# Kernel optimization log

Hardware: AMD Instinct MI355X
Metric: run time of the kernel (lower is better)

The kernel has to match this reference:

```python
import jax, jax.numpy as jnp
import numpy as np

EMBED = 512
HEADS = 8
FMUL = 4
TAU = 2.0
V_TH = 1.0      # spiking threshold (spikingjelly default)
ALPHA = 2.0     # ATan surrogate alpha (spikingjelly default)
EPS = 1e-5


@jax.custom_vjp
def spike_fn(v):
    # Heaviside spike with ATan surrogate gradient (spikingjelly surrogate.ATan)
    return (v >= V_TH).astype(v.dtype)

def _spike_fwd(v):
    return spike_fn(v), v

def _spike_bwd(v, g):
    t = (jnp.pi / 2.0) * ALPHA * (v - V_TH)
    return (g * (ALPHA / 2.0) / (1.0 + t * t),)

spike_fn.defvjp(_spike_fwd, _spike_bwd)


def layernorm(x, g, b):
    mu = jnp.mean(x, axis=-1, keepdims=True)
    var = jnp.mean(jnp.square(x - mu), axis=-1, keepdims=True)
    return (x - mu) * jax.lax.rsqrt(var + EPS) * g + b


def setup_inputs() -> dict:
    key = jax.random.key(0)
    ks = jax.random.split(key, 12)
    m, s, e = 4, 2048, EMBED
    f = e * FMUL
    sc = 0.02
    return {
        "x":  jax.random.normal(ks[0], (m, s, e), jnp.float32),
        "wq": jax.random.normal(ks[1], (e, e), jnp.float32) * sc,
        "bq": jnp.zeros((e,), jnp.float32),
        "wk": jax.random.normal(ks[2], (e, e), jnp.float32) * sc,
        "bk": jnp.zeros((e,), jnp.float32),
        "wv": jax.random.normal(ks[3], (e, e), jnp.float32) * sc,
        "bv": jnp.zeros((e,), jnp.float32),
        "w1": jax.random.normal(ks[4], (e, f), jnp.float32) * sc,
        "b1": jnp.zeros((f,), jnp.float32),
        "w2": jax.random.normal(ks[5], (f, e), jnp.float32) * sc,
        "b2": jnp.zeros((e,), jnp.float32),
        "g1": jnp.ones((e,), jnp.float32),
        "be1": jnp.zeros((e,), jnp.float32),
        "g2": jnp.ones((e,), jnp.float32),
        "be2": jnp.zeros((e,), jnp.float32),
    }


def reference(x, wq, bq, wk, bk, wv, bv, w1, b1, w2, b2, g1, be1, g2, be2):
    m, s, e = x.shape
    h = HEADS
    d = e // h

    # --- pre-norm attention (NOTE: original has NO 1/sqrt(d) scaling) ---
    n1 = layernorm(x, g1, be1)
    q = (n1 @ wq + bq).reshape(m, s, h, d).transpose(0, 2, 1, 3)  # [m,h,s,d]
    k = (n1 @ wk + bk).reshape(m, s, h, d).transpose(0, 2, 1, 3)
    v = (n1 @ wv + bv).reshape(m, s, h, d).transpose(0, 2, 1, 3)
    scores = jnp.einsum('bhqd,bhkd->bhqk', q, k)       # [m,h,s,s], unscaled
    attn = jax.nn.softmax(scores, axis=-1)
    ctx = jnp.einsum('bhqk,bhkd->bhqd', attn, v)       # [m,h,s,d]
    att_out = ctx.transpose(0, 2, 1, 3).reshape(m, s, e)

    x = x + att_out
    # dropout p=0.4 is identity at inference (eval path in the original)

    # --- FFN with spiking activation ---
    n2 = layernorm(x, g2, be2)
    h1 = n2 @ w1 + b1                                  # [m,s,4e]
    # single-step LIF charge from v=0: v = v + (x - v)/tau = x/tau
    spikes = spike_fn(h1 / TAU)
    return x + (spikes @ w2 + b2)
```

## Files before the change

### kernel.cpp

```cpp
#include <hip/hip_runtime.h>
#include <stdint.h>

#define EMB 512
#define SEQ 2048
#define MB 4
#define NH 8
#define HD 64
#define ROWS (MB*SEQ)
#define MARGIN 0.02f
#define CAP 65536
#define LOG2E 1.44269504f
#define EXPB (-17.3123405f)

typedef unsigned short u16;
typedef __attribute__((ext_vector_type(8))) short bf16x8;
typedef __attribute__((ext_vector_type(4))) float f32x4;
typedef __attribute__((ext_vector_type(2))) unsigned int u32x2;
typedef __attribute__((ext_vector_type(4))) unsigned int u32x4;

union Frag { u32x2 u[2]; bf16x8 v; };
union Frag4 { unsigned u[4]; bf16x8 v; };

__device__ __forceinline__ u16 f2bf(float f) {
  union { float f; unsigned u; } a; a.f = f;
  unsigned r = a.u + 0x7FFFu + ((a.u >> 16) & 1u);
  return (u16)(r >> 16);
}
__device__ __forceinline__ float bflo(unsigned u) {
  union { unsigned u; float f; } c; c.u = u << 16; return c.f;
}
__device__ __forceinline__ float bfhi(unsigned u) {
  union { unsigned u; float f; } c; c.u = u & 0xffff0000u; return c.f;
}
__device__ __forceinline__ void gld16(const void* g, void* l) {
  __builtin_amdgcn_global_load_lds(
      (const __attribute__((address_space(1))) void*)g,
      (__attribute__((address_space(3))) void*)l, 16, 0, 0);
}


__global__ __launch_bounds__(256) void k_prep(
    const float* __restrict__ x, const float* __restrict__ g1, const float* __restrict__ be1,
    const float* __restrict__ wq, const float* __restrict__ wk,
    const float* __restrict__ wv, const float* __restrict__ w1,
    u16* __restrict__ n1, u16* __restrict__ wqkvT, u16* __restrict__ w1T,
    int* __restrict__ cnt) {
  __shared__ float tile[32][33];
  int b = blockIdx.x, tid = threadIdx.x;
  if (b < 1792) {
    const float* src; u16* dst; int N, bx, by;
    if (b < 768) {
      int z = b >> 8, rem = b & 255; bx = rem & 15; by = rem >> 4; N = 512;
      src = (z == 0) ? wq : ((z == 1) ? wk : wv);
      dst = wqkvT + z * 512 * 512;
    } else {
      int rem = b - 768; bx = rem & 63; by = rem >> 6; N = 2048;
      src = w1; dst = w1T;
    }
    int tx = tid & 31, ty = tid >> 5;
    int k0 = by * 32, n0 = bx * 32;
    for (int i = 0; i < 32; i += 8)
      tile[ty + i][tx] = src[(size_t)(k0 + ty + i) * N + n0 + tx];
    __syncthreads();
    for (int i = 0; i < 32; i += 8)
      dst[(size_t)(n0 + ty + i) * 512 + k0 + tx] = f2bf(tile[tx][ty + i]);
  } else {
    if (b == 1792 && tid < 2) cnt[tid] = 0;
    int wid = tid >> 6, lane = tid & 63;
    int row = (b - 1792) * 4 + wid;
    const float* xr = x + (size_t)row * EMB + lane * 8;
    f32x4 v0 = *(const f32x4*)xr;
    f32x4 v1 = *(const f32x4*)(xr + 4);
    float s = v0.x+v0.y+v0.z+v0.w + v1.x+v1.y+v1.z+v1.w;
    float q = v0.x*v0.x+v0.y*v0.y+v0.z*v0.z+v0.w*v0.w
            + v1.x*v1.x+v1.y*v1.y+v1.z*v1.z+v1.w*v1.w;
    #pragma unroll
    for (int o = 1; o < 64; o <<= 1) { s += __shfl_xor(s, o); q += __shfl_xor(q, o); }
    float mu = s * (1.0f/512.0f);
    float rs = 1.0f / sqrtf(q * (1.0f/512.0f) - mu*mu + 1e-5f);
    f32x4 ga = *(const f32x4*)(g1 + lane*8), gb = *(const f32x4*)(g1 + lane*8 + 4);
    f32x4 ba = *(const f32x4*)(be1 + lane*8), bb = *(const f32x4*)(be1 + lane*8 + 4);
    union { u16 h[8]; u32x4 v; } o8;
    o8.h[0] = f2bf((v0.x-mu)*rs*ga.x + ba.x); o8.h[1] = f2bf((v0.y-mu)*rs*ga.y + ba.y);
    o8.h[2] = f2bf((v0.z-mu)*rs*ga.z + ba.z); o8.h[3] = f2bf((v0.w-mu)*rs*ga.w + ba.w);
    o8.h[4] = f2bf((v1.x-mu)*rs*gb.x + bb.x); o8.h[5] = f2bf((v1.y-mu)*rs*gb.y + bb.y);
    o8.h[6] = f2bf((v1.z-mu)*rs*gb.z + bb.z); o8.h[7] = f2bf((v1.w-mu)*rs*gb.w + bb.w);
    *(u32x4*)(n1 + (size_t)row * EMB + lane * 8) = o8.v;
  }
}

__global__ __launch_bounds__(256) void k_ln2(const float* __restrict__ x,
    const u16* __restrict__ att, const float* __restrict__ g, const float* __restrict__ b,
    const float* __restrict__ b2, float* __restrict__ x2, u16* __restrict__ n2,
    float* __restrict__ out) {
  int wid = threadIdx.x >> 6, lane = threadIdx.x & 63;
  int row = blockIdx.x * 4 + wid;
  size_t base = (size_t)row * EMB + lane * 8;
  u32x4 av = *(const u32x4*)(att + base);
  f32x4 t0, t1;
  t0.x = bflo(av.x); t0.y = bfhi(av.x); t0.z = bflo(av.y); t0.w = bfhi(av.y);
  t1.x = bflo(av.z); t1.y = bfhi(av.z); t1.z = bflo(av.w); t1.w = bfhi(av.w);
  f32x4 v0 = *(const f32x4*)(x + base)     + t0;
  f32x4 v1 = *(const f32x4*)(x + base + 4) + t1;
  *(f32x4*)(x2 + base) = v0;
  *(f32x4*)(x2 + base + 4) = v1;
  *(f32x4*)(out + base)     = v0 + *(const f32x4*)(b2 + lane*8);
  *(f32x4*)(out + base + 4) = v1 + *(const f32x4*)(b2 + lane*8 + 4);
  float s = v0.x+v0.y+v0.z+v0.w + v1.x+v1.y+v1.z+v1.w;
  float q = v0.x*v0.x+v0.y*v0.y+v0.z*v0.z+v0.w*v0.w
          + v1.x*v1.x+v1.y*v1.y+v1.z*v1.z+v1.w*v1.w;
  #pragma unroll
  for (int o = 1; o < 64; o <<= 1) { s += __shfl_xor(s, o); q += __shfl_xor(q, o); }
  float mu = s * (1.0f/512.0f);
  float rs = 1.0f / sqrtf(q * (1.0f/512.0f) - mu*mu + 1e-5f);
  f32x4 ga = *(const f32x4*)(g + lane*8), gb = *(const f32x4*)(g + lane*8 + 4);
  f32x4 ba = *(const f32x4*)(b + lane*8), bb = *(const f32x4*)(b + lane*8 + 4);
  union { u16 h[8]; u32x4 v; } o8;
  o8.h[0] = f2bf((v0.x-mu)*rs*ga.x + ba.x); o8.h[1] = f2bf((v0.y-mu)*rs*ga.y + ba.y);
  o8.h[2] = f2bf((v0.z-mu)*rs*ga.z + ba.z); o8.h[3] = f2bf((v0.w-mu)*rs*ga.w + ba.w);
  o8.h[4] = f2bf((v1.x-mu)*rs*gb.x + bb.x); o8.h[5] = f2bf((v1.y-mu)*rs*gb.y + bb.y);
  o8.h[6] = f2bf((v1.z-mu)*rs*gb.z + bb.z); o8.h[7] = f2bf((v1.w-mu)*rs*gb.w + bb.w);
  *(u32x4*)(n2 + (size_t)row * EMB + lane * 8) = o8.v;
}

#define GEMM_CORE(A_, Bt_, m0_, n0_)                                           \
  __shared__ u16 As[2][128 * 32];                                              \
  __shared__ u16 Bs[2][128 * 32];                                              \
  int tid = threadIdx.x;                                                       \
  int wid = tid >> 6, lane = tid & 63;                                         \
  int quad = lane >> 4, ln15 = lane & 15;                                      \
  int wm = (wid >> 1) * 64, wn = (wid & 1) * 64;                               \
  int arow = lane >> 2, acol = (lane & 3) * 8;                                 \
  const u16* gA0 = A_  + (size_t)(m0_ + wid * 32 + arow) * 512 + acol;         \
  const u16* gA1 = gA0 + (size_t)16 * 512;                                     \
  const u16* gB0 = Bt_ + (size_t)(n0_ + wid * 32 + arow) * 512 + acol;         \
  const u16* gB1 = gB0 + (size_t)16 * 512;                                     \
  f32x4 acc[4][4] = {};                                                        \
  gld16(gA0, &As[0][(wid * 32) * 32]); gld16(gA1, &As[0][(wid * 32 + 16) * 32]);\
  gld16(gB0, &Bs[0][(wid * 32) * 32]); gld16(gB1, &Bs[0][(wid * 32 + 16) * 32]);\
  for (int kt = 0; kt < 16; kt++) {                                            \
    int cur = kt & 1;                                                          \
    __syncthreads();                                                           \
    if (kt < 15) {                                                             \
      int ko = (kt + 1) * 32;                                                  \
      gld16(gA0 + ko, &As[cur ^ 1][(wid * 32) * 32]);                          \
      gld16(gA1 + ko, &As[cur ^ 1][(wid * 32 + 16) * 32]);                     \
      gld16(gB0 + ko, &Bs[cur ^ 1][(wid * 32) * 32]);                          \
      gld16(gB1 + ko, &Bs[cur ^ 1][(wid * 32 + 16) * 32]);                     \
    }                                                                          \
    bf16x8 af[4], bf[4];                                                       \
    _Pragma("unroll")                                                          \
    for (int i = 0; i < 4; i++) {                                              \
      af[i] = *(const bf16x8*)&As[cur][(wm + i * 16 + ln15) * 32 + quad * 8];  \
      bf[i] = *(const bf16x8*)&Bs[cur][(wn + i * 16 + ln15) * 32 + quad * 8];  \
    }                                                                          \
    _Pragma("unroll")                                                          \
    for (int i = 0; i < 4; i++)                                                \
      _Pragma("unroll")                                                        \
      for (int j = 0; j < 4; j++)                                              \
        acc[i][j] = __builtin_amdgcn_mfma_f32_16x16x32_bf16(af[i], bf[j],      \
                                                            acc[i][j], 0, 0, 0);\
  }                                                                            \
  __syncthreads();

__global__ __launch_bounds__(256) void k_gemm_qkv(
    const u16* __restrict__ A, const u16* __restrict__ Bt,
    const float* __restrict__ bq, const float* __restrict__ bk, const float* __restrict__ bv,
    u16* __restrict__ Qb, u16* __restrict__ Kb, u16* __restrict__ Vtb) {
  int bid = blockIdx.x + 12 * blockIdx.y;
  int c = bid & 7, r = bid >> 3;
  int m0 = (c * 8 + r / 12) * 128, n0 = (r % 12) * 128;
  GEMM_CORE(A, Bt, m0, n0)
  #pragma unroll
  for (int j = 0; j < 4; j++) {
    int n = n0 + wn + j * 16 + ln15;
    int t = n >> 9, cc = n & 511, head = cc >> 6, dd = cc & 63;
    float bias = (t == 0) ? bq[cc] : ((t == 1) ? bk[cc] : bv[cc]);
    #pragma unroll
    for (int i = 0; i < 4; i++) {
      int row0 = m0 + wm + i * 16 + quad * 4;
      int mm = row0 >> 11, ss0 = row0 & 2047;
      if (t == 2) {
        union { u16 h[4]; u32x2 v; } pk;
        #pragma unroll
        for (int r2 = 0; r2 < 4; r2++) pk.h[r2] = f2bf(acc[i][j][r2] + bias);
        *(u32x2*)(Vtb + ((size_t)(mm * 8 + head) * 64 + dd) * 2048 + ss0) = pk.v;
      } else {
        u16* dst = (t == 0) ? Qb : Kb;
        #pragma unroll
        for (int r2 = 0; r2 < 4; r2++)
          dst[((size_t)(mm * 8 + head) * 2048 + ss0 + r2) * 64 + dd] =
              f2bf(acc[i][j][r2] + bias);
      }
    }
  }
}

__global__ __launch_bounds__(256) void k_gemm_ffn1(
    const u16* __restrict__ A, const u16* __restrict__ Bt, const float* __restrict__ b1,
    int* __restrict__ cnt, unsigned* __restrict__ spikeL, unsigned* __restrict__ candL) {
  int bid = blockIdx.x + 16 * blockIdx.y;
  int c = bid & 7, r = bid >> 3;
  int m0 = (c * 8 + r / 16) * 128, n0 = (r % 16) * 128;
  GEMM_CORE(A, Bt, m0, n0)
  #pragma unroll
  for (int j = 0; j < 4; j++) {
    int n = n0 + wn + j * 16 + ln15;
    float bias = b1[n];
    #pragma unroll
    for (int i = 0; i < 4; i++) {
      #pragma unroll
      for (int r2 = 0; r2 < 4; r2++) {
        int row = m0 + wm + i * 16 + quad * 4 + r2;
        float hv = acc[i][j][r2] + bias;
        if (hv >= 2.0f - MARGIN) {
          if (hv >= 2.0f + MARGIN) {
            int ix = atomicAdd(&cnt[0], 1);
            if (ix < CAP) spikeL[ix] = (unsigned)(row * 2048 + n);
          } else {
            int ix = atomicAdd(&cnt[1], 1);
            if (ix < CAP) candL[ix] = (unsigned)(row * 2048 + n);
          }
        }
      }
    }
  }
}

#define F_STAGE(BUF, T0)                                                       \
  do {                                                                         \
    gld16(gK0 + (size_t)(T0)       * 4096, &L.SB[BUF][0][0][rb0 * 64]);        \
    gld16(gK1 + (size_t)(T0)       * 4096, &L.SB[BUF][0][0][rb1 * 64]);        \
    gld16(gK0 + (size_t)((T0) + 1) * 4096, &L.SB[BUF][0][1][rb0 * 64]);        \
    gld16(gK1 + (size_t)((T0) + 1) * 4096, &L.SB[BUF][0][1][rb1 * 64]);        \
    gld16(gV0 + (T0) * 64,       &L.SB[BUF][1][0][rb0 * 64]);                  \
    gld16(gV1 + (T0) * 64,       &L.SB[BUF][1][0][rb1 * 64]);                  \
    gld16(gV0 + ((T0) + 1) * 64, &L.SB[BUF][1][1][rb0 * 64]);                  \
    gld16(gV1 + ((T0) + 1) * 64, &L.SB[BUF][1][1][rb1 * 64]);                  \
  } while (0)

#define F_INNER(BUF, SUB)                                                      \
  do {                                                                         \
    const u16* Kc = L.SB[BUF][0][SUB];                                         \
    const u16* Vc = L.SB[BUF][1][SUB];                                         \
    f32x4 s4[2][4];                                                            \
    __builtin_amdgcn_s_setprio(1);                                             \
    _Pragma("unroll")                                                          \
    for (int j = 0; j < 4; j++) {                                              \
      bf16x8 a = *(const bf16x8*)(Kc + (j * 16 + ln15) * 64 + ((quad ^ lm) * 8)); \
      s4[0][j] = __builtin_amdgcn_mfma_f32_16x16x32_bf16(a, aQ[0][0].v, z4, 0, 0, 0); \
      s4[1][j] = __builtin_amdgcn_mfma_f32_16x16x32_bf16(a, aQ[1][0].v, z4, 0, 0, 0); \
    }                                                                          \
    _Pragma("unroll")                                                          \
    for (int j = 0; j < 4; j++) {                                              \
      bf16x8 a = *(const bf16x8*)(Kc + (j * 16 + ln15) * 64 + (((4 + quad) ^ lm) * 8)); \
      s4[0][j] = __builtin_amdgcn_mfma_f32_16x16x32_bf16(a, aQ[0][1].v, s4[0][j], 0, 0, 0); \
      s4[1][j] = __builtin_amdgcn_mfma_f32_16x16x32_bf16(a, aQ[1][1].v, s4[1][j], 0, 0, 0); \
    }                                                                          \
    __builtin_amdgcn_s_setprio(0);                                             \
    Frag4 bP[2][2];                                                            \
    _Pragma("unroll")                                                          \
    for (int h = 0; h < 2; h++) {                                              \
      unsigned pr[4][4];                                                       \
      _Pragma("unroll")                                                        \
      for (int j = 0; j < 4; j++)                                              \
        _Pragma("unroll")                                                      \
        for (int r = 0; r < 4; r++) {                                          \
          float p = __builtin_amdgcn_exp2f(fmaf(s4[h][j][r], LOG2E, EXPB));    \
          union { float f; unsigned u; } cc; cc.f = p;                         \
          pr[j][r] = cc.u;                                                     \
        }                                                                      \
      _Pragma("unroll")                                                        \
      for (int t = 0; t < 2; t++) {                                            \
        bP[h][t].u[0] = __builtin_amdgcn_perm(pr[2*t][1],   pr[2*t][0],   0x07060302u); \
        bP[h][t].u[1] = __builtin_amdgcn_perm(pr[2*t][3],   pr[2*t][2],   0x07060302u); \
        bP[h][t].u[2] = __builtin_amdgcn_perm(pr[2*t+1][1], pr[2*t+1][0], 0x07060302u); \
        bP[h][t].u[3] = __builtin_amdgcn_perm(pr[2*t+1][3], pr[2*t+1][2], 0x07060302u); \
      }                                                                        \
    }                                                                          \
    __builtin_amdgcn_s_setprio(1);                                             \
    lacc[0] = __builtin_amdgcn_mfma_f32_16x16x32_bf16(vOne.v, bP[0][0].v, lacc[0], 0, 0, 0); \
    lacc[1] = __builtin_amdgcn_mfma_f32_16x16x32_bf16(vOne.v, bP[1][0].v, lacc[1], 0, 0, 0); \
    lacc[0] = __builtin_amdgcn_mfma_f32_16x16x32_bf16(vOne.v, bP[0][1].v, lacc[0], 0, 0, 0); \
    lacc[1] = __builtin_amdgcn_mfma_f32_16x16x32_bf16(vOne.v, bP[1][1].v, lacc[1], 0, 0, 0); \
    _Pragma("unroll")                                                          \
    for (int t = 0; t < 2; t++)                                                \
      _Pragma("unroll")                                                        \
      for (int j = 0; j < 4; j++) {                                            \
        int row = j * 16 + ln15;                                               \
        int c0 = 4 * t + (quad >> 1), sub = (quad & 1) * 4;                    \
        Frag aV;                                                               \
        aV.u[0] = *(const u32x2*)(Vc + row * 64 + ((c0 ^ lm) * 8) + sub);      \
        aV.u[1] = *(const u32x2*)(Vc + row * 64 + (((c0 + 2) ^ lm) * 8) + sub);\
        U[0][j] = __builtin_amdgcn_mfma_f32_16x16x32_bf16(aV.v, bP[0][t].v,    \
                                                          U[0][j], 0, 0, 0);   \
        U[1][j] = __builtin_amdgcn_mfma_f32_16x16x32_bf16(aV.v, bP[1][t].v,    \
                                                          U[1][j], 0, 0, 0);   \
      }                                                                        \
    __builtin_amdgcn_s_setprio(0);                                             \
  } while (0)

#define F_STEP(CUR, S)                                                         \
  do {                                                                         \
    __syncthreads();                                                           \
    if ((S) < 15) F_STAGE((CUR) ^ 1, 2 * (S) + 2);                             \
    F_INNER(CUR, 0);                                                           \
    F_INNER(CUR, 1);                                                           \
  } while (0)

__global__ __launch_bounds__(256, 2) void k_flash(
    const u16* __restrict__ Q, const u16* __restrict__ K,
    const u16* __restrict__ Vt, u16* __restrict__ att) {
  __shared__ union {
    u16 SB[2][2][2][64 * 64];
    float T[4][16 * 68];
  } L;
  int tid = threadIdx.x, wid = tid >> 6, lane = tid & 63;
  int quad = lane >> 4, ln15 = lane & 15, lm = ln15 & 7;
  int bid = blockIdx.x + 16 * (blockIdx.y + 8 * (int)blockIdx.z);
  int swz = (bid & 7) * 64 + (bid >> 3);
  int qb = swz & 15, head = (swz >> 4) & 7, mm = swz >> 7;
  int mh = mm * 8 + head;
  const u16* Qp = Q  + (size_t)mh * SEQ * HD;
  const u16* Kp = K  + (size_t)mh * SEQ * HD;
  const u16* Vp = Vt + (size_t)mh * HD * SEQ;
  int q0 = qb * 128 + wid * 32;

  Frag aQ[2][2];
  #pragma unroll
  for (int h = 0; h < 2; h++)
    #pragma unroll
    for (int t = 0; t < 2; t++) {
      u32x4 g = *(const u32x4*)(Qp + (size_t)(q0 + h * 16 + ln15) * 64 + t * 32 + quad * 8);
      aQ[h][t].u[0].x = g.x; aQ[h][t].u[0].y = g.y;
      aQ[h][t].u[1].x = g.z; aQ[h][t].u[1].y = g.w;
    }
  const f32x4 z4 = {0.f, 0.f, 0.f, 0.f};
  Frag4 vOne;
  vOne.u[0] = 0x3F803F80u; vOne.u[1] = 0x3F803F80u;
  vOne.u[2] = 0x3F803F80u; vOne.u[3] = 0x3F803F80u;

  int srow = lane >> 3;
  int sch  = (lane & 7) ^ (srow & 7);
  int rb0 = wid * 16, rb1 = wid * 16 + 8;
  const u16* gK0 = Kp + (size_t)(rb0 + srow) * 64 + sch * 8;
  const u16* gK1 = Kp + (size_t)(rb1 + srow) * 64 + sch * 8;
  const u16* gV0 = Vp + (size_t)(rb0 + srow) * SEQ + sch * 8;
  const u16* gV1 = Vp + (size_t)(rb1 + srow) * SEQ + sch * 8;

  f32x4 lacc[2] = {};
  f32x4 U[2][4] = {};

  F_STAGE(0, 0);
  for (int it = 0; it < 8; it++) {
    F_STEP(0, 2 * it);
    F_STEP(1, 2 * it + 1);
  }
  __syncthreads();

  #pragma unroll
  for (int h = 0; h < 2; h++) {
    float rl = 1.0f / lacc[h][0];
    float* Tw = L.T[wid];
    #pragma unroll
    for (int j = 0; j < 4; j++)
      *(f32x4*)(Tw + ln15 * 68 + j * 16 + quad * 4) = U[h][j] * rl;
    #pragma unroll
    for (int s = 0; s < 4; s++) {
      f32x4 o = *(const f32x4*)(Tw + (quad * 4 + s) * 68 + ln15 * 4);
      union { u16 h4[4]; u32x2 v; } pk;
      pk.h4[0] = f2bf(o.x); pk.h4[1] = f2bf(o.y);
      pk.h4[2] = f2bf(o.z); pk.h4[3] = f2bf(o.w);
      *(u32x2*)(att + ((size_t)mm * SEQ + q0 + h * 16 + quad * 4 + s) * EMB +
                head * 64 + ln15 * 4) = pk.v;
    }
  }
}

__global__ __launch_bounds__(256) void k_fixup(
    const float* __restrict__ x2, const float* __restrict__ w1, const float* __restrict__ b1,
    const float* __restrict__ g2, const float* __restrict__ be2,
    int* __restrict__ cnt, unsigned* __restrict__ spikeL, const unsigned* __restrict__ candL) {
  __shared__ float sb[8];
  int tid = threadIdx.x;
  int nC = cnt[1]; if (nC > CAP) nC = CAP;
  for (int e = blockIdx.x; e < nC; e += gridDim.x) {
    unsigned v = candL[e];
    int row = (int)(v >> 11), col = (int)(v & 2047u);
    const float* xr = x2 + (size_t)row * 512;
    float x0 = xr[tid], x1 = xr[tid + 256];
    float s = x0 + x1, q = x0 * x0 + x1 * x1;
    #pragma unroll
    for (int o = 1; o < 64; o <<= 1) { s += __shfl_xor(s, o); q += __shfl_xor(q, o); }
    if ((tid & 63) == 0) { sb[tid >> 6] = s; sb[4 + (tid >> 6)] = q; }
    __syncthreads();
    float st = sb[0] + sb[1] + sb[2] + sb[3];
    float qt = sb[4] + sb[5] + sb[6] + sb[7];
    __syncthreads();
    float mu = st * (1.f / 512.f);
    float rs = 1.f / sqrtf(qt * (1.f / 512.f) - mu * mu + 1e-5f);
    float na = (x0 - mu) * rs * g2[tid] + be2[tid];
    float nb = (x1 - mu) * rs * g2[tid + 256] + be2[tid + 256];
    float dd = na * w1[(size_t)tid * 2048 + col] + nb * w1[(size_t)(tid + 256) * 2048 + col];
    #pragma unroll
    for (int o = 1; o < 64; o <<= 1) dd += __shfl_xor(dd, o);
    if ((tid & 63) == 0) sb[tid >> 6] = dd;
    __syncthreads();
    if (tid == 0) {
      float hv = sb[0] + sb[1] + sb[2] + sb[3] + b1[col];
      if (hv >= 2.0f) { int ix = atomicAdd(&cnt[0], 1); if (ix < CAP) spikeL[ix] = v; }
    }
    __syncthreads();
  }
}

__global__ void k_apply(const float* __restrict__ w2, const int* __restrict__ cnt,
                        const unsigned* __restrict__ spikeL, float* __restrict__ out) {
  int n = cnt[0]; if (n > CAP) n = CAP;
  int tid = threadIdx.x;
  for (int e = blockIdx.x; e < n; e += gridDim.x) {
    unsigned v = spikeL[e];
    int row = (int)(v >> 11), col = (int)(v & 2047u);
    atomicAdd(&out[(size_t)row * 512 + tid * 2 + 0], w2[(size_t)col * 512 + tid * 2 + 0]);
    atomicAdd(&out[(size_t)row * 512 + tid * 2 + 1], w2[(size_t)col * 512 + tid * 2 + 1]);
  }
}


extern "C" void kernel_launch(void* const* d_in, const int* in_sizes, int n_in,
                              void* d_out, int out_size, void* d_ws, size_t ws_size,
                              hipStream_t stream) {
  (void)in_sizes; (void)n_in; (void)out_size; (void)ws_size;
  const float* x   = (const float*)d_in[0];
  const float* wq  = (const float*)d_in[1];
  const float* bq  = (const float*)d_in[2];
  const float* wk  = (const float*)d_in[3];
  const float* bk  = (const float*)d_in[4];
  const float* wv  = (const float*)d_in[5];
  const float* bv  = (const float*)d_in[6];
  const float* w1  = (const float*)d_in[7];
  const float* b1  = (const float*)d_in[8];
  const float* w2  = (const float*)d_in[9];
  const float* b2  = (const float*)d_in[10];
  const float* g1  = (const float*)d_in[11];
  const float* be1 = (const float*)d_in[12];
  const float* g2  = (const float*)d_in[13];
  const float* be2 = (const float*)d_in[14];
  float* out = (float*)d_out;

  char* w = (char*)d_ws;
  size_t off = 0;
  auto take = [&](size_t bytes) { char* p = w + off; off += (bytes + 255) & ~(size_t)255; return p; };
  int*      cnt    = (int*)take(256);
  u16*      n1     = (u16*)take((size_t)ROWS * EMB * 2);
  u16*      wqkvT  = (u16*)take((size_t)1536 * 512 * 2);
  u16*      w1T    = (u16*)take((size_t)2048 * 512 * 2);
  u16*      Qb     = (u16*)take((size_t)MB * NH * SEQ * HD * 2);
  u16*      Kb     = (u16*)take((size_t)MB * NH * SEQ * HD * 2);
  u16*      Vtb    = (u16*)take((size_t)MB * NH * SEQ * HD * 2);
  u16*      att    = (u16*)take((size_t)ROWS * EMB * 2);
  float*    x2     = (float*)take((size_t)ROWS * EMB * 4);
  u16*      n2     = (u16*)take((size_t)ROWS * EMB * 2);
  unsigned* spikeL = (unsigned*)take((size_t)CAP * 4);
  unsigned* candL  = (unsigned*)take((size_t)CAP * 4);

  k_prep<<<3840, 256, 0, stream>>>(x, g1, be1, wq, wk, wv, w1, n1, wqkvT, w1T, cnt);
  k_gemm_qkv<<<dim3(12, 64), 256, 0, stream>>>(n1, wqkvT, bq, bk, bv, Qb, Kb, Vtb);
  k_flash<<<dim3(16, 8, 4), 256, 0, stream>>>(Qb, Kb, Vtb, att);
  k_ln2<<<ROWS / 4, 256, 0, stream>>>(x, att, g2, be2, b2, x2, n2, out);
  k_gemm_ffn1<<<dim3(16, 64), 256, 0, stream>>>(n2, w1T, b1, cnt, spikeL, candL);
  k_fixup<<<256, 256, 0, stream>>>(x2, w1, b1, g2, be2, cnt, spikeL, candL);
  k_apply<<<128, 256, 0, stream>>>(w2, cnt, spikeL, out);
}
```

Measured before the change: 199.1 us.

## Fold log2e into K weights and exp bias into MFMA accumulator; drop x2 buffer

Scales the K projection weights and bias by log2(e) during prep, and seeds the QK^T MFMA accumulator with the constant exp offset. The softmax exponent then becomes a bare exp2 with no per-element FMA. Separately, k_ln2 no longer writes the fp32 residual x2; the fixup kernel recomputes it from x plus the bf16 attention output. This removes one full-size fp32 store at the cost of extra loads in the sparse fixup. Scaling K before bf16 rounding changes rounding slightly.

```diff
diff --git a/kernel.cpp b/kernel.cpp
--- a/kernel.cpp
+++ b/kernel.cpp
@@ -32,6 +32,9 @@
 __device__ __forceinline__ float bfhi(unsigned u) {
   union { unsigned u; float f; } c; c.u = u & 0xffff0000u; return c.f;
 }
+__device__ __forceinline__ float b2f(u16 h) {
+  union { unsigned u; float f; } c; c.u = (unsigned)h << 16; return c.f;
+}
 __device__ __forceinline__ void gld16(const void* g, void* l) {
   __builtin_amdgcn_global_load_lds(
       (const __attribute__((address_space(1))) void*)g,
@@ -49,9 +52,11 @@
   int b = blockIdx.x, tid = threadIdx.x;
   if (b < 1792) {
     const float* src; u16* dst; int N, bx, by;
+    float scl = 1.0f;
     if (b < 768) {
       int z = b >> 8, rem = b & 255; bx = rem & 15; by = rem >> 4; N = 512;
       src = (z == 0) ? wq : ((z == 1) ? wk : wv);
+      if (z == 1) scl = LOG2E;
       dst = wqkvT + z * 512 * 512;
     } else {
       int rem = b - 768; bx = rem & 63; by = rem >> 6; N = 2048;
@@ -63,7 +68,7 @@
       tile[ty + i][tx] = src[(size_t)(k0 + ty + i) * N + n0 + tx];
     __syncthreads();
     for (int i = 0; i < 32; i += 8)
-      dst[(size_t)(n0 + ty + i) * 512 + k0 + tx] = f2bf(tile[tx][ty + i]);
+      dst[(size_t)(n0 + ty + i) * 512 + k0 + tx] = f2bf(tile[tx][ty + i] * scl);
   } else {
     if (b == 1792 && tid < 2) cnt[tid] = 0;
     int wid = tid >> 6, lane = tid & 63;
@@ -91,7 +96,7 @@
 
 __global__ __launch_bounds__(256) void k_ln2(const float* __restrict__ x,
     const u16* __restrict__ att, const float* __restrict__ g, const float* __restrict__ b,
-    const float* __restrict__ b2, float* __restrict__ x2, u16* __restrict__ n2,
+    const float* __restrict__ b2, u16* __restrict__ n2,
     float* __restrict__ out) {
   int wid = threadIdx.x >> 6, lane = threadIdx.x & 63;
   int row = blockIdx.x * 4 + wid;
@@ -102,8 +107,6 @@
   t1.x = bflo(av.z); t1.y = bfhi(av.z); t1.z = bflo(av.w); t1.w = bfhi(av.w);
   f32x4 v0 = *(const f32x4*)(x + base)     + t0;
   f32x4 v1 = *(const f32x4*)(x + base + 4) + t1;
-  *(f32x4*)(x2 + base) = v0;
-  *(f32x4*)(x2 + base + 4) = v1;
   *(f32x4*)(out + base)     = v0 + *(const f32x4*)(b2 + lane*8);
   *(f32x4*)(out + base + 4) = v1 + *(const f32x4*)(b2 + lane*8 + 4);
   float s = v0.x+v0.y+v0.z+v0.w + v1.x+v1.y+v1.z+v1.w;
@@ -175,7 +178,7 @@
   for (int j = 0; j < 4; j++) {
     int n = n0 + wn + j * 16 + ln15;
     int t = n >> 9, cc = n & 511, head = cc >> 6, dd = cc & 63;
-    float bias = (t == 0) ? bq[cc] : ((t == 1) ? bk[cc] : bv[cc]);
+    float bias = (t == 0) ? bq[cc] : ((t == 1) ? bk[cc] * LOG2E : bv[cc]);
     #pragma unroll
     for (int i = 0; i < 4; i++) {
       int row0 = m0 + wm + i * 16 + quad * 4;
@@ -248,8 +251,8 @@
     _Pragma("unroll")                                                          \
     for (int j = 0; j < 4; j++) {                                              \
       bf16x8 a = *(const bf16x8*)(Kc + (j * 16 + ln15) * 64 + ((quad ^ lm) * 8)); \
-      s4[0][j] = __builtin_amdgcn_mfma_f32_16x16x32_bf16(a, aQ[0][0].v, z4, 0, 0, 0); \
-      s4[1][j] = __builtin_amdgcn_mfma_f32_16x16x32_bf16(a, aQ[1][0].v, z4, 0, 0, 0); \
+      s4[0][j] = __builtin_amdgcn_mfma_f32_16x16x32_bf16(a, aQ[0][0].v, e4, 0, 0, 0); \
+      s4[1][j] = __builtin_amdgcn_mfma_f32_16x16x32_bf16(a, aQ[1][0].v, e4, 0, 0, 0); \
     }                                                                          \
     _Pragma("unroll")                                                          \
     for (int j = 0; j < 4; j++) {                                              \
@@ -266,7 +269,7 @@
       for (int j = 0; j < 4; j++)                                              \
         _Pragma("unroll")                                                      \
         for (int r = 0; r < 4; r++) {                                          \
-          float p = __builtin_amdgcn_exp2f(fmaf(s4[h][j][r], LOG2E, EXPB));    \
+          float p = __builtin_amdgcn_exp2f(s4[h][j][r]);                       \
           union { float f; unsigned u; } cc; cc.f = p;                         \
           pr[j][r] = cc.u;                                                     \
         }                                                                      \
@@ -335,7 +338,7 @@
       aQ[h][t].u[0].x = g.x; aQ[h][t].u[0].y = g.y;
       aQ[h][t].u[1].x = g.z; aQ[h][t].u[1].y = g.w;
     }
-  const f32x4 z4 = {0.f, 0.f, 0.f, 0.f};
+  const f32x4 e4 = {EXPB, EXPB, EXPB, EXPB};
   Frag4 vOne;
   vOne.u[0] = 0x3F803F80u; vOne.u[1] = 0x3F803F80u;
   vOne.u[2] = 0x3F803F80u; vOne.u[3] = 0x3F803F80u;
@@ -378,7 +381,8 @@
 }
 
 __global__ __launch_bounds__(256) void k_fixup(
-    const float* __restrict__ x2, const float* __restrict__ w1, const float* __restrict__ b1,
+    const float* __restrict__ x, const u16* __restrict__ att,
+    const float* __restrict__ w1, const float* __restrict__ b1,
     const float* __restrict__ g2, const float* __restrict__ be2,
     int* __restrict__ cnt, unsigned* __restrict__ spikeL, const unsigned* __restrict__ candL) {
   __shared__ float sb[8];
@@ -387,8 +391,10 @@
   for (int e = blockIdx.x; e < nC; e += gridDim.x) {
     unsigned v = candL[e];
     int row = (int)(v >> 11), col = (int)(v & 2047u);
-    const float* xr = x2 + (size_t)row * 512;
-    float x0 = xr[tid], x1 = xr[tid + 256];
+    const float* xr = x + (size_t)row * 512;
+    const u16* ar = att + (size_t)row * 512;
+    float x0 = xr[tid] + b2f(ar[tid]);
+    float x1 = xr[tid + 256] + b2f(ar[tid + 256]);
     float s = x0 + x1, q = x0 * x0 + x1 * x1;
     #pragma unroll
     for (int o = 1; o < 64; o <<= 1) { s += __shfl_xor(s, o); q += __shfl_xor(q, o); }
@@ -459,7 +465,6 @@
   u16*      Kb     = (u16*)take((size_t)MB * NH * SEQ * HD * 2);
   u16*      Vtb    = (u16*)take((size_t)MB * NH * SEQ * HD * 2);
   u16*      att    = (u16*)take((size_t)ROWS * EMB * 2);
-  float*    x2     = (float*)take((size_t)ROWS * EMB * 4);
   u16*      n2     = (u16*)take((size_t)ROWS * EMB * 2);
   unsigned* spikeL = (unsigned*)take((size_t)CAP * 4);
   unsigned* candL  = (unsigned*)take((size_t)CAP * 4);
@@ -467,8 +472,8 @@
   k_prep<<<3840, 256, 0, stream>>>(x, g1, be1, wq, wk, wv, w1, n1, wqkvT, w1T, cnt);
   k_gemm_qkv<<<dim3(12, 64), 256, 0, stream>>>(n1, wqkvT, bq, bk, bv, Qb, Kb, Vtb);
   k_flash<<<dim3(16, 8, 4), 256, 0, stream>>>(Qb, Kb, Vtb, att);
-  k_ln2<<<ROWS / 4, 256, 0, stream>>>(x, att, g2, be2, b2, x2, n2, out);
+  k_ln2<<<ROWS / 4, 256, 0, stream>>>(x, att, g2, be2, b2, n2, out);
   k_gemm_ffn1<<<dim3(16, 64), 256, 0, stream>>>(n2, w1T, b1, cnt, spikeL, candL);
-  k_fixup<<<256, 256, 0, stream>>>(x2, w1, b1, g2, be2, cnt, spikeL, candL);
+  k_fixup<<<256, 256, 0, stream>>>(x, att, w1, b1, g2, be2, cnt, spikeL, candL);
   k_apply<<<128, 256, 0, stream>>>(w2, cnt, spikeL, out);
 }
```

Measured after the change: 195.0 us (median of 3 runs). -2.0%, faster.
